# Kernel tuning notes

Measured on AMD Instinct MI355X. Metric: run time of the kernel, lower is better.

The kernel has to match this reference:

```python
import jax, jax.numpy as jnp
import numpy as np

WIN = 11
K1 = 0.01
K2 = 0.03


def setup_inputs() -> dict:
    key = jax.random.key(0)
    k1, k2 = jax.random.split(key)
    B, C, H, W = 64, 1, 512, 512
    img = jax.random.uniform(k1, (B, C, H, W), dtype=jnp.float32)
    ref = jax.random.uniform(k2, (B, C, H, W), dtype=jnp.float32)
    data_range = jnp.ones((B,), dtype=jnp.float32)
    return {"img": img, "ref": ref, "data_range": data_range}


def _box_filter(x, win):
    w = jnp.ones((1, 1, win, win), dtype=x.dtype) / (win * win)
    pad = win // 2
    return jax.lax.conv_general_dilated(
        x, w, window_strides=(1, 1),
        padding=[(pad, pad), (pad, pad)],
        dimension_numbers=("NCHW", "OIHW", "NCHW"))


def reference(img, ref, data_range):
    dr = data_range[:, None, None, None]
    C1 = (K1 * dr) ** 2
    C2 = (K2 * dr) ** 2
    n_pix = WIN * WIN
    cov_norm = n_pix / (n_pix - 1)

    ux = _box_filter(img, WIN)
    uy = _box_filter(ref, WIN)
    uxx = _box_filter(img * img, WIN)
    uyy = _box_filter(ref * ref, WIN)
    uxy = _box_filter(img * ref, WIN)

    vx = cov_norm * (uxx - ux * ux)
    vy = cov_norm * (uyy - uy * uy)
    vxy = cov_norm * (uxy - ux * uy)

    A1 = 2 * ux * uy + C1
    A2 = 2 * vxy + C2
    B1 = ux ** 2 + uy ** 2 + C1
    B2 = vx + vy + C2
    S = A1 * A2 / (B1 * B2)
    return S
```

## Files before the change

kernel.cpp:

```cpp
#include <hip/hip_runtime.h>


static constexpr int HI = 512, WI = 512;
static constexpr int RS = 8;
static constexpr int STRIPS = HI / RS;

__device__ __forceinline__ void horiz11(const float v[8], float H[8], int lane) {
  float L[5], R[5];
#pragma unroll
  for (int k = 0; k < 5; ++k) {
    float lt = __shfl(v[3 + k], (lane + 63) & 63);
    L[k] = (lane == 0) ? 0.f : lt;
    float rt = __shfl(v[k], (lane + 1) & 63);
    R[k] = (lane == 63) ? 0.f : rt;
  }
  float h = (((L[0] + L[1]) + (L[2] + L[3])) + ((L[4] + v[0]) + (v[1] + v[2])))
            + ((v[3] + v[4]) + v[5]);
  H[0] = h;
  h = h - L[0] + v[6]; H[1] = h;
  h = h - L[1] + v[7]; H[2] = h;
  h = h - L[2] + R[0]; H[3] = h;
  h = h - L[3] + R[1]; H[4] = h;
  h = h - L[4] + R[2]; H[5] = h;
  h = h - v[0] + R[3]; H[6] = h;
  h = h - v[1] + R[4]; H[7] = h;
}

__global__ __launch_bounds__(256, 3)
void ssim_wave(const float* __restrict__ img, const float* __restrict__ ref,
               const float* __restrict__ drng, float* __restrict__ out)
{
  const int lane = threadIdx.x & 63;
  const int wv   = (int)blockIdx.x * 4 + (threadIdx.x >> 6);
  const int b    = wv >> 6;
  const int r0   = (wv & (STRIPS - 1)) * RS;
  const int c0   = lane * 8;

  const float dr  = drng[b];
  const float C1  = (0.01f * dr) * (0.01f * dr);
  const float C2  = (0.03f * dr) * (0.03f * dr);
  const float inv_n    = 1.0f / 121.0f;
  const float cov_norm = 121.0f / 120.0f;

  const size_t base = (size_t)b * ((size_t)HI * WI);
  const float* xb = img + base;
  const float* yb = ref + base;
  float*       ob = out + base;

  float Sx[8], Sy[8], Sxx[8], Syy[8], Sxy[8];
#pragma unroll
  for (int c = 0; c < 8; ++c) { Sx[c]=0.f; Sy[c]=0.f; Sxx[c]=0.f; Syy[c]=0.f; Sxy[c]=0.f; }

  for (int i = 0; i < RS + 10; ++i) {
    const int ri = r0 - 5 + i;
    float xn[8], yn[8], xo[8], yo[8];

    if (ri >= 0 && ri < HI) {
      const float4* px = (const float4*)(xb + (size_t)ri * WI + c0);
      const float4* py = (const float4*)(yb + (size_t)ri * WI + c0);
      const float4 a0 = px[0], a1 = px[1];
      const float4 b0 = py[0], b1 = py[1];
      xn[0]=a0.x; xn[1]=a0.y; xn[2]=a0.z; xn[3]=a0.w;
      xn[4]=a1.x; xn[5]=a1.y; xn[6]=a1.z; xn[7]=a1.w;
      yn[0]=b0.x; yn[1]=b0.y; yn[2]=b0.z; yn[3]=b0.w;
      yn[4]=b1.x; yn[5]=b1.y; yn[6]=b1.z; yn[7]=b1.w;
    } else {
#pragma unroll
      for (int c = 0; c < 8; ++c) { xn[c]=0.f; yn[c]=0.f; }
    }

    const int rold = ri - 11;
    if (i >= 11 && rold >= 0) {
      const float4* px = (const float4*)(xb + (size_t)rold * WI + c0);
      const float4* py = (const float4*)(yb + (size_t)rold * WI + c0);
      const float4 a0 = px[0], a1 = px[1];
      const float4 b0 = py[0], b1 = py[1];
      xo[0]=a0.x; xo[1]=a0.y; xo[2]=a0.z; xo[3]=a0.w;
      xo[4]=a1.x; xo[5]=a1.y; xo[6]=a1.z; xo[7]=a1.w;
      yo[0]=b0.x; yo[1]=b0.y; yo[2]=b0.z; yo[3]=b0.w;
      yo[4]=b1.x; yo[5]=b1.y; yo[6]=b1.z; yo[7]=b1.w;
    } else {
#pragma unroll
      for (int c = 0; c < 8; ++c) { xo[c]=0.f; yo[c]=0.f; }
    }

#pragma unroll
    for (int c = 0; c < 8; ++c) {
      Sx[c]  += xn[c] - xo[c];
      Sy[c]  += yn[c] - yo[c];
      Sxx[c] = fmaf(xn[c], xn[c], fmaf(-xo[c], xo[c], Sxx[c]));
      Syy[c] = fmaf(yn[c], yn[c], fmaf(-yo[c], yo[c], Syy[c]));
      Sxy[c] = fmaf(xn[c], yn[c], fmaf(-xo[c], yo[c], Sxy[c]));
    }

    if (i >= 10) {
      float H0[8], H1[8], H2[8], H3[8], H4[8];
      horiz11(Sx,  H0, lane);
      horiz11(Sy,  H1, lane);
      horiz11(Sxx, H2, lane);
      horiz11(Syy, H3, lane);
      horiz11(Sxy, H4, lane);

      float res[8];
#pragma unroll
      for (int c = 0; c < 8; ++c) {
        const float ux  = H0[c] * inv_n, uy  = H1[c] * inv_n;
        const float uxx = H2[c] * inv_n, uyy = H3[c] * inv_n, uxy = H4[c] * inv_n;
        const float vx  = cov_norm * (uxx - ux * ux);
        const float vy  = cov_norm * (uyy - uy * uy);
        const float vxy = cov_norm * (uxy - ux * uy);
        const float A1 = 2.f * ux * uy + C1;
        const float A2 = 2.f * vxy + C2;
        const float B1 = ux * ux + uy * uy + C1;
        const float B2 = vx + vy + C2;
        res[c] = (A1 * A2) * __builtin_amdgcn_rcpf(B1 * B2);
      }
      const int ro = ri - 5;
      float4* po = (float4*)(ob + (size_t)ro * WI + c0);
      po[0] = make_float4(res[0], res[1], res[2], res[3]);
      po[1] = make_float4(res[4], res[5], res[6], res[7]);
    }
  }
}

extern "C" void kernel_launch(void* const* d_in, const int* in_sizes, int n_in,
                              void* d_out, int out_size, void* d_ws, size_t ws_size,
                              hipStream_t stream)
{
  const float* img = (const float*)d_in[0];
  const float* ref = (const float*)d_in[1];
  const float* drg = (const float*)d_in[2];
  float* out = (float*)d_out;
  const int B = in_sizes[0] / (HI * WI);
  const int waves = B * STRIPS;
  dim3 grid(waves / 4);
  dim3 block(256);
  hipLaunchKernelGGL(ssim_wave, grid, block, 0, stream, img, ref, drg, out);
}
```

Before: 210.9 us.

## Double-buffer row loads with zero-row pointer and taller strips

Strip height grows from 8 to 16 rows, so the 10-row vertical halo is re-read less often. Row loads for the entering and leaving rows are now prefetched two steps ahead into register double buffers. Out-of-range rows are redirected to a zeroed workspace row instead of branching, so the loads stay unconditional. The costs are more registers (launch bounds lowered to 2 blocks per SIMD target), an extra memset launch, and half as many waves in flight.

After: 199.7 us. -5.3%, faster.

```diff
diff --git a/kernel.cpp b/kernel.cpp
--- a/kernel.cpp
+++ b/kernel.cpp
@@ -2,8 +2,15 @@
 
 
 static constexpr int HI = 512, WI = 512;
-static constexpr int RS = 8;
-static constexpr int STRIPS = HI / RS;
+static constexpr int RS = 16;
+static constexpr int STEPS = RS + 10;
+static constexpr int SPB = HI / RS;
+
+struct R8 { float4 a, b; };
+
+__device__ __forceinline__ R8 ld8(const float* p) {
+  R8 r; r.a = ((const float4*)p)[0]; r.b = ((const float4*)p)[1]; return r;
+}
 
 __device__ __forceinline__ void horiz11(const float v[8], float H[8], int lane) {
   float L[5], R[5];
@@ -26,14 +33,15 @@
   h = h - v[1] + R[4]; H[7] = h;
 }
 
-__global__ __launch_bounds__(256, 3)
+__global__ __launch_bounds__(256, 2)
 void ssim_wave(const float* __restrict__ img, const float* __restrict__ ref,
-               const float* __restrict__ drng, float* __restrict__ out)
+               const float* __restrict__ drng, const float* __restrict__ zrow,
+               float* __restrict__ out)
 {
   const int lane = threadIdx.x & 63;
   const int wv   = (int)blockIdx.x * 4 + (threadIdx.x >> 6);
-  const int b    = wv >> 6;
-  const int r0   = (wv & (STRIPS - 1)) * RS;
+  const int b    = wv / SPB;
+  const int r0   = (wv % SPB) * RS;
   const int c0   = lane * 8;
 
   const float dr  = drng[b];
@@ -47,41 +55,38 @@
   const float* yb = ref + base;
   float*       ob = out + base;
 
+  auto nptr = [&](const float* tb, int i) -> const float* {
+    const int ri = r0 - 5 + i;
+    return (((unsigned)ri < (unsigned)HI) ? tb + (size_t)ri * WI : zrow) + c0;
+  };
+  auto optr = [&](const float* tb, int i) -> const float* {
+    const int ro = r0 - 16 + i;
+    return ((i >= 11 && ro >= 0) ? tb + (size_t)ro * WI : zrow) + c0;
+  };
+
   float Sx[8], Sy[8], Sxx[8], Syy[8], Sxy[8];
 #pragma unroll
   for (int c = 0; c < 8; ++c) { Sx[c]=0.f; Sy[c]=0.f; Sxx[c]=0.f; Syy[c]=0.f; Sxy[c]=0.f; }
 
-  for (int i = 0; i < RS + 10; ++i) {
-    const int ri = r0 - 5 + i;
-    float xn[8], yn[8], xo[8], yo[8];
+  R8 nx[2], ny[2], ox[2], oy[2];
+  nx[0]=ld8(nptr(xb,0)); ny[0]=ld8(nptr(yb,0)); ox[0]=ld8(optr(xb,0)); oy[0]=ld8(optr(yb,0));
+  nx[1]=ld8(nptr(xb,1)); ny[1]=ld8(nptr(yb,1)); ox[1]=ld8(optr(xb,1)); oy[1]=ld8(optr(yb,1));
 
-    if (ri >= 0 && ri < HI) {
-      const float4* px = (const float4*)(xb + (size_t)ri * WI + c0);
-      const float4* py = (const float4*)(yb + (size_t)ri * WI + c0);
-      const float4 a0 = px[0], a1 = px[1];
-      const float4 b0 = py[0], b1 = py[1];
-      xn[0]=a0.x; xn[1]=a0.y; xn[2]=a0.z; xn[3]=a0.w;
-      xn[4]=a1.x; xn[5]=a1.y; xn[6]=a1.z; xn[7]=a1.w;
-      yn[0]=b0.x; yn[1]=b0.y; yn[2]=b0.z; yn[3]=b0.w;
-      yn[4]=b1.x; yn[5]=b1.y; yn[6]=b1.z; yn[7]=b1.w;
-    } else {
-#pragma unroll
-      for (int c = 0; c < 8; ++c) { xn[c]=0.f; yn[c]=0.f; }
-    }
+#pragma unroll 2
+  for (int i = 0; i < STEPS; ++i) {
+    const int s = i & 1;
+    float xn[8] = { nx[s].a.x, nx[s].a.y, nx[s].a.z, nx[s].a.w,
+                    nx[s].b.x, nx[s].b.y, nx[s].b.z, nx[s].b.w };
+    float yn[8] = { ny[s].a.x, ny[s].a.y, ny[s].a.z, ny[s].a.w,
+                    ny[s].b.x, ny[s].b.y, ny[s].b.z, ny[s].b.w };
+    float xo[8] = { ox[s].a.x, ox[s].a.y, ox[s].a.z, ox[s].a.w,
+                    ox[s].b.x, ox[s].b.y, ox[s].b.z, ox[s].b.w };
+    float yo[8] = { oy[s].a.x, oy[s].a.y, oy[s].a.z, oy[s].a.w,
+                    oy[s].b.x, oy[s].b.y, oy[s].b.z, oy[s].b.w };
 
-    const int rold = ri - 11;
-    if (i >= 11 && rold >= 0) {
-      const float4* px = (const float4*)(xb + (size_t)rold * WI + c0);
-      const float4* py = (const float4*)(yb + (size_t)rold * WI + c0);
-      const float4 a0 = px[0], a1 = px[1];
-      const float4 b0 = py[0], b1 = py[1];
-      xo[0]=a0.x; xo[1]=a0.y; xo[2]=a0.z; xo[3]=a0.w;
-      xo[4]=a1.x; xo[5]=a1.y; xo[6]=a1.z; xo[7]=a1.w;
-      yo[0]=b0.x; yo[1]=b0.y; yo[2]=b0.z; yo[3]=b0.w;
-      yo[4]=b1.x; yo[5]=b1.y; yo[6]=b1.z; yo[7]=b1.w;
-    } else {
-#pragma unroll
-      for (int c = 0; c < 8; ++c) { xo[c]=0.f; yo[c]=0.f; }
+    if (i + 2 < STEPS) {
+      nx[s]=ld8(nptr(xb,i+2)); ny[s]=ld8(nptr(yb,i+2));
+      ox[s]=ld8(optr(xb,i+2)); oy[s]=ld8(optr(yb,i+2));
     }
 
 #pragma unroll
@@ -115,7 +120,7 @@
         const float B2 = vx + vy + C2;
         res[c] = (A1 * A2) * __builtin_amdgcn_rcpf(B1 * B2);
       }
-      const int ro = ri - 5;
+      const int ro = r0 + i - 10;
       float4* po = (float4*)(ob + (size_t)ro * WI + c0);
       po[0] = make_float4(res[0], res[1], res[2], res[3]);
       po[1] = make_float4(res[4], res[5], res[6], res[7]);
@@ -131,9 +136,13 @@
   const float* ref = (const float*)d_in[1];
   const float* drg = (const float*)d_in[2];
   float* out = (float*)d_out;
+
+  hipMemsetAsync(d_ws, 0, (size_t)WI * sizeof(float) + 64, stream);
+
   const int B = in_sizes[0] / (HI * WI);
-  const int waves = B * STRIPS;
+  const int waves = B * SPB;
   dim3 grid(waves / 4);
   dim3 block(256);
-  hipLaunchKernelGGL(ssim_wave, grid, block, 0, stream, img, ref, drg, out);
+  hipLaunchKernelGGL(ssim_wave, grid, block, 0, stream,
+                     img, ref, drg, (const float*)d_ws, out);
 }
```
